# Performance work log

Measured on AMD Instinct MI355X. Metric: run time of the kernel, lower is better.

## Reference

```python
import jax, jax.numpy as jnp
import numpy as np

KH, KW = 3, 3
DIL = 1
PH = DIL * (KH - 1) // 2
PW = DIL * (KW - 1) // 2


def setup_inputs() -> dict:
    key = jax.random.key(0)
    kq, kk = jax.random.split(key)
    B, C, H, W = 8, 128, 128, 128
    Q = jax.random.normal(kq, (B, C, H, W), dtype=jnp.float32)
    K = jax.random.normal(kk, (B, C, H, W), dtype=jnp.float32)
    return {"Q": Q, "K": K}


def reference(Q, K):
    # output[b, i*KW+j, h, w] = sum_c Q[b,c,h,w] * K_padded[b,c,h+i*DIL, w+j*DIL]
    B, C, H, W = Q.shape
    Kp = jnp.pad(K, ((0, 0), (0, 0), (PH, PH), (PW, PW)))
    outs = []
    for i in range(KH):
        for j in range(KW):
            Ks = Kp[:, :, i * DIL:i * DIL + H, j * DIL:j * DIL + W]  # shifted K window
            outs.append(jnp.sum(Q * Ks, axis=1))  # reduce over channels -> (B,H,W)
    return jnp.stack(outs, axis=1)  # (B, KH*KW, H, W)
```

## Files before the change

kernel.cpp:

```cpp
#include <hip/hip_runtime.h>


#define Bn 8
#define Cn 128
#define Hn 128
#define Wn 128
#define HWn (Hn * Wn)

__global__ __launch_bounds__(256) void msa_conv_kernel(
    const float* __restrict__ Q, const float* __restrict__ K,
    float* __restrict__ out) {
  const int w = threadIdx.x;
  const int h = blockIdx.x * 2 + threadIdx.y;
  const int b = blockIdx.y;

  const bool wm  = (w > 0), wp  = (w < Wn - 1);
  const bool hmv = (h > 0), hpv = (h < Hn - 1);

  const int hm = hmv ? h - 1 : h + 1;
  const int hp = hpv ? h + 1 : h - 1;
  const int dm = wm ? -1 : +1;
  const int dp = wp ? +1 : -1;

  const size_t bk = (size_t)b * Cn * HWn;
  const float* q  = Q + bk + (size_t)h * Wn + w;
  const float* km = K + bk + (size_t)hm * Wn + w;
  const float* k0 = K + bk + (size_t)h  * Wn + w;
  const float* kp = K + bk + (size_t)hp * Wn + w;
  const float* kmL = km + dm; const float* kmR = km + dp;
  const float* k0L = k0 + dm; const float* k0R = k0 + dp;
  const float* kpL = kp + dm; const float* kpR = kp + dp;

  float a00 = 0.f, a01 = 0.f, a02 = 0.f;
  float a10 = 0.f, a11 = 0.f, a12 = 0.f;
  float a20 = 0.f, a21 = 0.f, a22 = 0.f;

#pragma unroll 4
  for (int c = 0; c < Cn; ++c) {
    const float qv = *q;
    const float m0 = *kmL, m1 = *km, m2 = *kmR;
    const float z0 = *k0L, z1 = *k0, z2 = *k0R;
    const float p0 = *kpL, p1 = *kp, p2 = *kpR;
    a00 += qv * m0; a01 += qv * m1; a02 += qv * m2;
    a10 += qv * z0; a11 += qv * z1; a12 += qv * z2;
    a20 += qv * p0; a21 += qv * p1; a22 += qv * p2;
    q += HWn;
    km += HWn; kmL += HWn; kmR += HWn;
    k0 += HWn; k0L += HWn; k0R += HWn;
    kp += HWn; kpL += HWn; kpR += HWn;
  }

  float res[9];
  res[0] = (hmv && wm) ? a00 : 0.f;
  res[1] = hmv ? a01 : 0.f;
  res[2] = (hmv && wp) ? a02 : 0.f;
  res[3] = wm ? a10 : 0.f;
  res[4] = a11;
  res[5] = wp ? a12 : 0.f;
  res[6] = (hpv && wm) ? a20 : 0.f;
  res[7] = hpv ? a21 : 0.f;
  res[8] = (hpv && wp) ? a22 : 0.f;

  float* o = out + (size_t)b * 9 * HWn + (size_t)h * Wn + w;
#pragma unroll
  for (int t = 0; t < 9; ++t) {
    *o = res[t];
    o += HWn;
  }
}

extern "C" void kernel_launch(void* const* d_in, const int* in_sizes, int n_in,
                              void* d_out, int out_size, void* d_ws,
                              size_t ws_size, hipStream_t stream) {
  const float* Q = (const float*)d_in[0];
  const float* K = (const float*)d_in[1];
  float* out = (float*)d_out;

  dim3 block(128, 2);
  dim3 grid(Hn / 2, Bn);
  msa_conv_kernel<<<grid, block, 0, stream>>>(Q, K, out);
}
```

Before: 156.2 us.

## Split channel reduction across blocks with workspace partials and reduce pass

Splits the 128-channel reduction into 4 chunks along a new grid z dimension, raising the block count from 512 to 2048 so more of the GPU's CUs are occupied. Each chunk writes partial outputs to a workspace, and a separate float4 kernel sums the four partials. If the workspace is too small, it zeroes the output and accumulates with atomics instead. The cost is extra launches and about 4x the output-sized traffic through the workspace.

```diff
diff --git a/kernel.cpp b/kernel.cpp
--- a/kernel.cpp
+++ b/kernel.cpp
@@ -6,13 +6,18 @@
 #define Hn 128
 #define Wn 128
 #define HWn (Hn * Wn)
+#define CSPLIT 4
+#define CCHUNK (Cn / CSPLIT)
+#define OUTN (Bn * 9 * HWn)
 
-__global__ __launch_bounds__(256) void msa_conv_kernel(
+template <bool ATOMIC>
+__global__ __launch_bounds__(256) void msa_conv_part(
     const float* __restrict__ Q, const float* __restrict__ K,
-    float* __restrict__ out) {
-  const int w = threadIdx.x;
-  const int h = blockIdx.x * 2 + threadIdx.y;
-  const int b = blockIdx.y;
+    float* __restrict__ dst) {
+  const int w  = threadIdx.x;
+  const int h  = blockIdx.x * 2 + threadIdx.y;
+  const int b  = blockIdx.y;
+  const int cs = blockIdx.z;
 
   const bool wm  = (w > 0), wp  = (w < Wn - 1);
   const bool hmv = (h > 0), hpv = (h < Hn - 1);
@@ -22,7 +27,7 @@
   const int dm = wm ? -1 : +1;
   const int dp = wp ? +1 : -1;
 
-  const size_t bk = (size_t)b * Cn * HWn;
+  const size_t bk = (size_t)b * Cn * HWn + (size_t)cs * CCHUNK * HWn;
   const float* q  = Q + bk + (size_t)h * Wn + w;
   const float* km = K + bk + (size_t)hm * Wn + w;
   const float* k0 = K + bk + (size_t)h  * Wn + w;
@@ -36,7 +41,7 @@
   float a20 = 0.f, a21 = 0.f, a22 = 0.f;
 
 #pragma unroll 4
-  for (int c = 0; c < Cn; ++c) {
+  for (int c = 0; c < CCHUNK; ++c) {
     const float qv = *q;
     const float m0 = *kmL, m1 = *km, m2 = *kmR;
     const float z0 = *k0L, z1 = *k0, z2 = *k0R;
@@ -61,12 +66,41 @@
   res[7] = hpv ? a21 : 0.f;
   res[8] = (hpv && wp) ? a22 : 0.f;
 
-  float* o = out + (size_t)b * 9 * HWn + (size_t)h * Wn + w;
+  const size_t o = (size_t)b * 9 * HWn + (size_t)h * Wn + w;
+  if (ATOMIC) {
 #pragma unroll
-  for (int t = 0; t < 9; ++t) {
-    *o = res[t];
-    o += HWn;
+    for (int t = 0; t < 9; ++t)
+      atomicAdd(dst + o + (size_t)t * HWn, res[t]);
+  } else {
+    float* p = dst + (size_t)cs * OUTN + o;
+#pragma unroll
+    for (int t = 0; t < 9; ++t) {
+      *p = res[t];
+      p += HWn;
+    }
   }
+}
+
+__global__ __launch_bounds__(256) void msa_reduce4(
+    const float* __restrict__ part, float* __restrict__ out) {
+  const int i = blockIdx.x * 256 + threadIdx.x;
+  const float4* p = (const float4*)part;
+  const int n4 = OUTN / 4;
+  float4 s0 = p[i];
+  float4 s1 = p[n4 + i];
+  float4 s2 = p[2 * n4 + i];
+  float4 s3 = p[3 * n4 + i];
+  float4 r;
+  r.x = (s0.x + s1.x) + (s2.x + s3.x);
+  r.y = (s0.y + s1.y) + (s2.y + s3.y);
+  r.z = (s0.z + s1.z) + (s2.z + s3.z);
+  r.w = (s0.w + s1.w) + (s2.w + s3.w);
+  ((float4*)out)[i] = r;
+}
+
+__global__ __launch_bounds__(256) void msa_zero(float* __restrict__ out) {
+  const int i = blockIdx.x * 256 + threadIdx.x;
+  ((float4*)out)[i] = make_float4(0.f, 0.f, 0.f, 0.f);
 }
 
 extern "C" void kernel_launch(void* const* d_in, const int* in_sizes, int n_in,
@@ -77,6 +111,15 @@
   float* out = (float*)d_out;
 
   dim3 block(128, 2);
-  dim3 grid(Hn / 2, Bn);
-  msa_conv_kernel<<<grid, block, 0, stream>>>(Q, K, out);
+  dim3 grid(Hn / 2, Bn, CSPLIT);
+
+  const size_t ws_need = (size_t)CSPLIT * OUTN * sizeof(float);
+  if (ws_size >= ws_need) {
+    float* part = (float*)d_ws;
+    msa_conv_part<false><<<grid, block, 0, stream>>>(Q, K, part);
+    msa_reduce4<<<OUTN / 4 / 256, 256, 0, stream>>>(part, out);
+  } else {
+    msa_zero<<<OUTN / 4 / 256, 256, 0, stream>>>(out);
+    msa_conv_part<true><<<grid, block, 0, stream>>>(Q, K, out);
+  }
 }
```

After: 157.4 us. No clear change (+0.8%).
